# Optimization experiments

Hardware: AMD Instinct MI355X
Metric: run time of the kernel (lower is better)

The kernel has to match this reference:

```python
import jax, jax.numpy as jnp
import numpy as np

H = 8          # num_heads
DK = 64        # head dim (head_size // num_heads)
SPARSITY = 0.5 # pre-softmax random drop probability
DROPOUT = 0.1  # post-softmax dropout probability


def setup_inputs() -> dict:
    key = jax.random.key(0)
    ks = jax.random.split(key, 12)
    B, S, D = 4, 2048, 512
    mk = lambda k, shp, scale=1.0: (jax.random.normal(k, shp, dtype=jnp.float32) * scale)
    return {
        "query": mk(ks[0], (B, S, D)),
        "key": mk(ks[1], (B, S, D)),
        "value": mk(ks[2], (B, S, D)),
        "Wq": mk(ks[3], (D, D), 0.04),
        "bq": mk(ks[4], (D,), 0.02),
        "Wk": mk(ks[5], (D, D), 0.04),
        "bk": mk(ks[6], (D,), 0.02),
        "Wv": mk(ks[7], (D, D), 0.04),
        "bv": mk(ks[8], (D,), 0.02),
        "Wo": mk(ks[9], (D, D), 0.04),
        "bo": mk(ks[10], (D,), 0.02),
    }


def _split_heads(x, B):
    # [B, S, H*DK] -> [B, H, S, DK]
    return x.reshape(B, -1, H, DK).transpose(0, 2, 1, 3)


def reference(query, key, value, Wq, bq, Wk, bk, Wv, bv, Wo, bo):
    B, S, D = query.shape
    # q/k/v projections (torch Linear: x @ W.T + b)
    q = _split_heads(query @ Wq.T + bq, B)   # [B, H, S, DK]
    k = _split_heads(key @ Wk.T + bk, B)
    v = _split_heads(value @ Wv.T + bv, B)

    scores = jnp.einsum("bhqd,bhkd->bhqk", q, k) / jnp.sqrt(jnp.float32(DK))

    # random pre-softmax sparsity mask: keep where U(0,1) > sparsity
    mkey = jax.random.fold_in(jax.random.key(42), 1)
    keep_sparse = jax.random.uniform(mkey, scores.shape) > SPARSITY
    scores = jnp.where(keep_sparse, scores, -jnp.inf)

    p_attn = jax.nn.softmax(scores, axis=-1)

    # dropout on attention probs, inverted scaling as in torch
    dkey = jax.random.fold_in(jax.random.key(42), 2)
    keep_drop = jax.random.uniform(dkey, p_attn.shape) >= DROPOUT
    p_attn = jnp.where(keep_drop, p_attn / (1.0 - DROPOUT), 0.0)

    x = jnp.einsum("bhqk,bhkd->bhqd", p_attn, v)        # [B, H, S, DK]
    x = x.transpose(0, 2, 1, 3).reshape(B, S, H * DK)    # [B, S, D]
    return x @ Wo.T + bo
```

## Files before the change

kernel.cpp:

```cpp
#include <hip/hip_runtime.h>
#include <stdint.h>

#define BATCH  4
#define SQ     2048
#define DMODEL 512
#define NH     8
#define DK     64

typedef __attribute__((ext_vector_type(8))) short short8;
typedef __attribute__((ext_vector_type(4))) float f32x4;

struct TFK { uint32_t a, b; };
constexpr uint32_t rotl_ce(uint32_t x, int d) {
  return (x << d) | (x >> (32 - d));
}
constexpr TFK tf_ce(uint32_t k0, uint32_t k1, uint32_t x0, uint32_t x1) {
  const uint32_t ks[3] = {k0, k1, k0 ^ k1 ^ 0x1BD11BDAu};
  const int rot[2][4] = {{13, 15, 26, 6}, {17, 29, 16, 24}};
  x0 += k0; x1 += k1;
  for (int c = 0; c < 5; ++c) {
    for (int j = 0; j < 4; ++j) {
      x0 += x1; x1 = rotl_ce(x1, rot[c & 1][j]); x1 ^= x0;
    }
    x0 += ks[(c + 1) % 3];
    x1 += ks[(c + 2) % 3] + (uint32_t)(c + 1);
  }
  return TFK{x0, x1};
}
constexpr TFK SPK = tf_ce(0u, 42u, 0u, 1u);
constexpr TFK DPK = tf_ce(0u, 42u, 0u, 2u);

template <uint32_t K0, uint32_t K1>
__device__ __forceinline__ uint32_t tf_bits(uint32_t ctr) {
  constexpr uint32_t KS2 = K0 ^ K1 ^ 0x1BD11BDAu;
  uint32_t x0 = K0;
  uint32_t x1 = K1 + ctr;
#define RND(d) { x0 += x1; x1 = __builtin_amdgcn_alignbit(x1, x1, 32 - (d)); x1 ^= x0; }
  RND(13) RND(15) RND(26) RND(6)
  x0 += K1; x1 += KS2 + 1u;
  RND(17) RND(29) RND(16) RND(24)
  x0 += KS2; x1 += K0 + 2u;
  RND(13) RND(15) RND(26) RND(6)
  x0 += K0; x1 += K1 + 3u;
  RND(17) RND(29) RND(16) RND(24)
  x0 += K1; x1 += KS2 + 4u;
  RND(13) RND(15) RND(26) RND(6)
  x0 += KS2; x1 += K0 + 5u;
#undef RND
  return x0 ^ x1;
}

#define SP_THR 0x80000200u
#define DP_THR 0x1999A200u

__device__ __forceinline__ ushort f2bf_rne(float f) {
  uint32_t u = __float_as_uint(f);
  return (ushort)((u + 0x7fffu + ((u >> 16) & 1u)) >> 16);
}

#define BM 64
#define BN 64
#define BK 32
template <int MODE>
__global__ __launch_bounds__(256) void proj_gemm_t(const float *__restrict__ X,
                                                   const float *__restrict__ W,
                                                   const float *__restrict__ bias,
                                                   void *__restrict__ Yv) {
  __shared__ __align__(16) uint8_t smem[17408];
  float (*Xs)[BM + 4] = (float (*)[BM + 4])smem;
  float (*Ws)[BN + 4] = (float (*)[BN + 4])(smem + 8704);
  const int bm = blockIdx.y * BM;
  const int bn = blockIdx.x * BN;
  const int tid = threadIdx.x;
  const int tx = tid & 15, ty = tid >> 4;
  float acc[4][4] = {};
  const int kk = tid & 31;
  const int r0 = tid >> 5;
  for (int k0 = 0; k0 < DMODEL; k0 += BK) {
#pragma unroll
    for (int p = 0; p < 8; ++p) {
      int r = r0 + p * 8;
      Xs[kk][r] = X[(size_t)(bm + r) * DMODEL + k0 + kk];
      Ws[kk][r] = W[(size_t)(bn + r) * DMODEL + k0 + kk];
    }
    __syncthreads();
#pragma unroll
    for (int k = 0; k < BK; ++k) {
      float4 a = *reinterpret_cast<const float4 *>(&Xs[k][ty * 4]);
      float4 b = *reinterpret_cast<const float4 *>(&Ws[k][tx * 4]);
      float av[4] = {a.x, a.y, a.z, a.w};
      float bv[4] = {b.x, b.y, b.z, b.w};
#pragma unroll
      for (int i = 0; i < 4; ++i)
#pragma unroll
        for (int j = 0; j < 4; ++j) acc[i][j] += av[i] * bv[j];
    }
    __syncthreads();
  }

  if (MODE == 0) {
    float *Y = (float *)Yv;
#pragma unroll
    for (int i = 0; i < 4; ++i) {
      const int m = bm + ty * 4 + i;
#pragma unroll
      for (int j = 0; j < 4; ++j) {
        const int n = bn + tx * 4 + j;
        Y[(size_t)m * DMODEL + n] = acc[i][j] + bias[n];
      }
    }
  } else if (MODE == 1) {
    ushort *Y = (ushort *)Yv;
#pragma unroll
    for (int i = 0; i < 4; ++i) {
      const int m = bm + ty * 4 + i;
      uint32_t u0 = f2bf_rne(acc[i][0] + bias[bn + tx * 4 + 0]);
      uint32_t u1 = f2bf_rne(acc[i][1] + bias[bn + tx * 4 + 1]);
      uint32_t u2 = f2bf_rne(acc[i][2] + bias[bn + tx * 4 + 2]);
      uint32_t u3 = f2bf_rne(acc[i][3] + bias[bn + tx * 4 + 3]);
      uint2 pk;
      pk.x = u0 | (u1 << 16);
      pk.y = u2 | (u3 << 16);
      *(uint2 *)&Y[(size_t)m * DMODEL + bn + tx * 4] = pk;
    }
  } else {
    ushort *T = (ushort *)smem;
#pragma unroll
    for (int i = 0; i < 4; ++i)
#pragma unroll
      for (int j = 0; j < 4; ++j) {
        const int nl = tx * 4 + j, ml = ty * 4 + i;
        T[nl * 72 + ml] = f2bf_rne(acc[i][j] + bias[bn + nl]);
      }
    __syncthreads();
    ushort *Y = (ushort *)Yv;
    const int row = tid >> 2, seg = tid & 3;
    uint4 a = *(uint4 *)&T[row * 72 + seg * 16];
    uint4 b2 = *(uint4 *)&T[row * 72 + seg * 16 + 8];
    const size_t gaddr =
        ((size_t)((bm >> 11) * 512 + bn + row)) * SQ + (bm & 2047) + seg * 16;
    *(uint4 *)&Y[gaddr] = a;
    *(uint4 *)&Y[gaddr + 8] = b2;
  }
}

__global__ __launch_bounds__(256, 2) void attn_mfma(
    const ushort *__restrict__ qp, const ushort *__restrict__ kp,
    const ushort *__restrict__ vpt, float *__restrict__ xa) {
  __shared__ __align__(16) uint8_t lds[24576];
  uint8_t *Ks = lds;
  uint8_t *Vt = lds + 8192;
  const int b = blockIdx.z, h = blockIdx.y;
  const int qb = blockIdx.x * 64;
  const int tid = threadIdx.x;
  const int w = tid >> 6, l = tid & 63;
  const int lr = l & 15, lq = l >> 4;
  uint8_t *Ps = lds + 16384 + w * 2048;
  const int bh = b * NH + h;

  short8 qf[2];
  {
    const int qrow = qb + w * 16 + lr;
    const ushort *qrowp = qp + ((size_t)(b * SQ + qrow)) * DMODEL + h * DK;
    qf[0] = *(const short8 *)(qrowp + lq * 8);
    qf[1] = *(const short8 *)(qrowp + 32 + lq * 8);
  }
  f32x4 o[4];
  f32x4 lacc;
#pragma unroll
  for (int nd = 0; nd < 4; ++nd) o[nd] = (f32x4){0.f, 0.f, 0.f, 0.f};
  lacc = (f32x4){0.f, 0.f, 0.f, 0.f};

  uint32_t rowflat[4];
#pragma unroll
  for (int r = 0; r < 4; ++r)
    rowflat[r] = ((uint32_t)(bh * SQ + qb + w * 16 + lq * 4 + r)) << 11;

  for (int kv = 0; kv < SQ; kv += 64) {
    __syncthreads();
    {
      const int row = tid >> 2;
      const int c0 = (tid & 3) * 2;
      const int sw = (row & 7) << 4;
      const ushort *ksrc =
          kp + ((size_t)(b * SQ + kv + row)) * DMODEL + h * DK + c0 * 8;
      uint4 d0 = *(const uint4 *)ksrc;
      uint4 d1 = *(const uint4 *)(ksrc + 8);
      *(uint4 *)(Ks + ((row * 128 + c0 * 16) ^ sw)) = d0;
      *(uint4 *)(Ks + ((row * 128 + (c0 + 1) * 16) ^ sw)) = d1;
      const ushort *vsrc = vpt + ((size_t)(bh * DK + row)) * SQ + kv + c0 * 8;
      uint4 e0 = *(const uint4 *)vsrc;
      uint4 e1 = *(const uint4 *)(vsrc + 8);
      *(uint4 *)(Vt + ((row * 128 + c0 * 16) ^ sw)) = e0;
      *(uint4 *)(Vt + ((row * 128 + (c0 + 1) * 16) ^ sw)) = e1;
    }
    __syncthreads();

    f32x4 s[4];
#pragma unroll
    for (int ni = 0; ni < 4; ++ni) s[ni] = (f32x4){0.f, 0.f, 0.f, 0.f};
#pragma unroll
    for (int ni = 0; ni < 4; ++ni) {
      const int krow = ni * 16 + lr;
      const int sw = (krow & 7) << 4;
#pragma unroll
      for (int kf = 0; kf < 2; ++kf) {
        short8 kb =
            *(const short8 *)(Ks + ((krow * 128 + kf * 64 + lq * 16) ^ sw));
        s[ni] = __builtin_amdgcn_mfma_f32_16x16x32_bf16(qf[kf], kb, s[ni], 0, 0, 0);
      }
    }

#pragma unroll
    for (int ni = 0; ni < 4; ++ni) {
#pragma unroll
      for (int r = 0; r < 4; ++r) {
        const uint32_t ctr = rowflat[r] + (uint32_t)(kv + ni * 16 + lr);
        const bool keep_s = tf_bits<SPK.a, SPK.b>(ctr) >= SP_THR;
        const bool keep_d = tf_bits<DPK.a, DPK.b>(ctr) >= DP_THR;
        float e = __expf(s[ni][r] * 0.125f);
        float p = keep_s ? e : 0.0f;
        lacc[r] += p;
        float pd = keep_d ? p * (1.0f / 0.9f) : 0.0f;
        const int prow = lq * 4 + r;
        *(ushort *)(Ps + ((prow * 128 + (ni * 16 + lr) * 2) ^ ((prow & 7) << 4))) =
            f2bf_rne(pd);
      }
    }

#pragma unroll
    for (int kf = 0; kf < 2; ++kf) {
      short8 pa = *(const short8 *)(Ps +
                                    ((lr * 128 + kf * 64 + lq * 16) ^ ((lr & 7) << 4)));
#pragma unroll
      for (int nd = 0; nd < 4; ++nd) {
        const int vrow = nd * 16 + lr;
        short8 vb = *(const short8 *)(Vt + ((vrow * 128 + kf * 64 + lq * 16) ^
                                            ((vrow & 7) << 4)));
        o[nd] = __builtin_amdgcn_mfma_f32_16x16x32_bf16(pa, vb, o[nd], 0, 0, 0);
      }
    }
  }

  float inv[4];
#pragma unroll
  for (int r = 0; r < 4; ++r) {
    float t = lacc[r];
    t += __shfl_xor(t, 1);
    t += __shfl_xor(t, 2);
    t += __shfl_xor(t, 4);
    t += __shfl_xor(t, 8);
    inv[r] = 1.0f / t;
  }
#pragma unroll
  for (int nd = 0; nd < 4; ++nd)
#pragma unroll
    for (int r = 0; r < 4; ++r) {
      const int qrow = qb + w * 16 + lq * 4 + r;
      xa[((size_t)(b * SQ + qrow)) * DMODEL + h * DK + nd * 16 + lr] =
          o[nd][r] * inv[r];
    }
}

extern "C" void kernel_launch(void *const *d_in, const int *in_sizes, int n_in,
                              void *d_out, int out_size, void *d_ws,
                              size_t ws_size, hipStream_t stream) {
  (void)in_sizes; (void)n_in; (void)out_size;
  const float *query = (const float *)d_in[0];
  const float *key_  = (const float *)d_in[1];
  const float *value = (const float *)d_in[2];
  const float *Wq = (const float *)d_in[3];
  const float *bq = (const float *)d_in[4];
  const float *Wk = (const float *)d_in[5];
  const float *bk = (const float *)d_in[6];
  const float *Wv = (const float *)d_in[7];
  const float *bv = (const float *)d_in[8];
  const float *Wo = (const float *)d_in[9];
  const float *bo = (const float *)d_in[10];
  float *out = (float *)d_out;

  const size_t MB = (size_t)1 << 20;
  if (ws_size < 40 * MB) return;

  char *ws = (char *)d_ws;
  ushort *qp  = (ushort *)(ws);
  ushort *kp  = (ushort *)(ws + 8 * MB);
  ushort *vpt = (ushort *)(ws + 16 * MB);
  float  *xa  = (float *)(ws + 24 * MB);

  dim3 gg(DMODEL / BN, (BATCH * SQ) / BM);
  proj_gemm_t<1><<<gg, 256, 0, stream>>>(query, Wq, bq, (void *)qp);
  proj_gemm_t<1><<<gg, 256, 0, stream>>>(key_, Wk, bk, (void *)kp);
  proj_gemm_t<2><<<gg, 256, 0, stream>>>(value, Wv, bv, (void *)vpt);

  attn_mfma<<<dim3(SQ / 64, NH, BATCH), 256, 0, stream>>>(qp, kp, vpt, xa);

  proj_gemm_t<0><<<gg, 256, 0, stream>>>(xa, Wo, bo, out);
}
```

Baseline: 794.0 us.

## Use split-bf16 MFMA GEMMs for projections instead of FP32 SIMT GEMMs

Replaces the four FP32 LDS-tiled SIMT projection GEMMs with MFMA bf16 GEMMs. Each FP32 operand is split into a high and a low bf16 part, and three MFMAs per tile approximate FP32 accuracy. New pre-pass kernels split the inputs and weights into these parts, and the attention kernel now writes its output as hi/lo bf16 pairs. The V projection is computed transposed by swapping operands. This adds extra memory traffic for the split passes and loads fragments straight from global memory without LDS staging.

```diff
diff --git a/kernel.cpp b/kernel.cpp
--- a/kernel.cpp
+++ b/kernel.cpp
@@ -57,96 +57,139 @@
   uint32_t u = __float_as_uint(f);
   return (ushort)((u + 0x7fffu + ((u >> 16) & 1u)) >> 16);
 }
-
-#define BM 64
-#define BN 64
-#define BK 32
+__device__ __forceinline__ float bf2f(ushort h) {
+  return __uint_as_float((uint32_t)h << 16);
+}
+
+__device__ __forceinline__ void split4(const float *__restrict__ src,
+                                       ushort *__restrict__ dh,
+                                       ushort *__restrict__ dl, size_t base) {
+  float4 x = *(const float4 *)(src + base);
+  uint32_t h[4], lo[4];
+#pragma unroll
+  for (int i = 0; i < 4; ++i) {
+    float xi = ((const float *)&x)[i];
+    ushort hh = f2bf_rne(xi);
+    h[i] = hh;
+    lo[i] = f2bf_rne(xi - bf2f(hh));
+  }
+  uint2 ph, pl;
+  ph.x = h[0] | (h[1] << 16);  ph.y = h[2] | (h[3] << 16);
+  pl.x = lo[0] | (lo[1] << 16); pl.y = lo[2] | (lo[3] << 16);
+  *(uint2 *)(dh + base) = ph;
+  *(uint2 *)(dl + base) = pl;
+}
+
+__global__ __launch_bounds__(256) void split_inputs_k(
+    const float *__restrict__ q, const float *__restrict__ k,
+    const float *__restrict__ v, ushort *__restrict__ qh,
+    ushort *__restrict__ ql, ushort *__restrict__ kh, ushort *__restrict__ kl,
+    ushort *__restrict__ vh, ushort *__restrict__ vl) {
+  const float *src = blockIdx.y == 0 ? q : (blockIdx.y == 1 ? k : v);
+  ushort *dh = blockIdx.y == 0 ? qh : (blockIdx.y == 1 ? kh : vh);
+  ushort *dl = blockIdx.y == 0 ? ql : (blockIdx.y == 1 ? kl : vl);
+  const size_t base = ((size_t)blockIdx.x * 256 + threadIdx.x) * 4;
+  split4(src, dh, dl, base);
+}
+
+__global__ __launch_bounds__(256) void split_w_k(
+    const float *__restrict__ w0, const float *__restrict__ w1,
+    const float *__restrict__ w2, const float *__restrict__ w3,
+    ushort *__restrict__ h0, ushort *__restrict__ l0, ushort *__restrict__ h1,
+    ushort *__restrict__ l1, ushort *__restrict__ h2, ushort *__restrict__ l2,
+    ushort *__restrict__ h3, ushort *__restrict__ l3) {
+  const int y = blockIdx.y;
+  const float *src = y == 0 ? w0 : (y == 1 ? w1 : (y == 2 ? w2 : w3));
+  ushort *dh = y == 0 ? h0 : (y == 1 ? h1 : (y == 2 ? h2 : h3));
+  ushort *dl = y == 0 ? l0 : (y == 1 ? l1 : (y == 2 ? l2 : l3));
+  const size_t base = ((size_t)blockIdx.x * 256 + threadIdx.x) * 4;
+  split4(src, dh, dl, base);
+}
+
 template <int MODE>
-__global__ __launch_bounds__(256) void proj_gemm_t(const float *__restrict__ X,
-                                                   const float *__restrict__ W,
-                                                   const float *__restrict__ bias,
-                                                   void *__restrict__ Yv) {
-  __shared__ __align__(16) uint8_t smem[17408];
-  float (*Xs)[BM + 4] = (float (*)[BM + 4])smem;
-  float (*Ws)[BN + 4] = (float (*)[BN + 4])(smem + 8704);
-  const int bm = blockIdx.y * BM;
-  const int bn = blockIdx.x * BN;
+__global__ __launch_bounds__(256) void proj_mfma(
+    const ushort *__restrict__ Ah, const ushort *__restrict__ Al,
+    const ushort *__restrict__ Bh, const ushort *__restrict__ Bl,
+    const float *__restrict__ bias, void *__restrict__ Yv) {
   const int tid = threadIdx.x;
-  const int tx = tid & 15, ty = tid >> 4;
-  float acc[4][4] = {};
-  const int kk = tid & 31;
-  const int r0 = tid >> 5;
-  for (int k0 = 0; k0 < DMODEL; k0 += BK) {
-#pragma unroll
-    for (int p = 0; p < 8; ++p) {
-      int r = r0 + p * 8;
-      Xs[kk][r] = X[(size_t)(bm + r) * DMODEL + k0 + kk];
-      Ws[kk][r] = W[(size_t)(bn + r) * DMODEL + k0 + kk];
-    }
-    __syncthreads();
-#pragma unroll
-    for (int k = 0; k < BK; ++k) {
-      float4 a = *reinterpret_cast<const float4 *>(&Xs[k][ty * 4]);
-      float4 b = *reinterpret_cast<const float4 *>(&Ws[k][tx * 4]);
-      float av[4] = {a.x, a.y, a.z, a.w};
-      float bv[4] = {b.x, b.y, b.z, b.w};
-#pragma unroll
-      for (int i = 0; i < 4; ++i)
-#pragma unroll
-        for (int j = 0; j < 4; ++j) acc[i][j] += av[i] * bv[j];
-    }
-    __syncthreads();
-  }
-
-  if (MODE == 0) {
-    float *Y = (float *)Yv;
-#pragma unroll
-    for (int i = 0; i < 4; ++i) {
-      const int m = bm + ty * 4 + i;
-#pragma unroll
-      for (int j = 0; j < 4; ++j) {
-        const int n = bn + tx * 4 + j;
-        Y[(size_t)m * DMODEL + n] = acc[i][j] + bias[n];
-      }
-    }
-  } else if (MODE == 1) {
-    ushort *Y = (ushort *)Yv;
-#pragma unroll
-    for (int i = 0; i < 4; ++i) {
-      const int m = bm + ty * 4 + i;
-      uint32_t u0 = f2bf_rne(acc[i][0] + bias[bn + tx * 4 + 0]);
-      uint32_t u1 = f2bf_rne(acc[i][1] + bias[bn + tx * 4 + 1]);
-      uint32_t u2 = f2bf_rne(acc[i][2] + bias[bn + tx * 4 + 2]);
-      uint32_t u3 = f2bf_rne(acc[i][3] + bias[bn + tx * 4 + 3]);
-      uint2 pk;
-      pk.x = u0 | (u1 << 16);
-      pk.y = u2 | (u3 << 16);
-      *(uint2 *)&Y[(size_t)m * DMODEL + bn + tx * 4] = pk;
-    }
-  } else {
-    ushort *T = (ushort *)smem;
-#pragma unroll
-    for (int i = 0; i < 4; ++i)
-#pragma unroll
-      for (int j = 0; j < 4; ++j) {
-        const int nl = tx * 4 + j, ml = ty * 4 + i;
-        T[nl * 72 + ml] = f2bf_rne(acc[i][j] + bias[bn + nl]);
-      }
-    __syncthreads();
-    ushort *Y = (ushort *)Yv;
-    const int row = tid >> 2, seg = tid & 3;
-    uint4 a = *(uint4 *)&T[row * 72 + seg * 16];
-    uint4 b2 = *(uint4 *)&T[row * 72 + seg * 16 + 8];
-    const size_t gaddr =
-        ((size_t)((bm >> 11) * 512 + bn + row)) * SQ + (bm & 2047) + seg * 16;
-    *(uint4 *)&Y[gaddr] = a;
-    *(uint4 *)&Y[gaddr + 8] = b2;
-  }
+  const int w = tid >> 6, l = tid & 63;
+  const int lr = l & 15, lq = l >> 4;
+  const int am = blockIdx.y * 128 + w * 32;
+  const int bn = blockIdx.x * 64;
+  f32x4 acc[2][4];
+#pragma unroll
+  for (int i = 0; i < 2; ++i)
+#pragma unroll
+    for (int j = 0; j < 4; ++j) acc[i][j] = (f32x4){0.f, 0.f, 0.f, 0.f};
+
+#pragma unroll 2
+  for (int k0 = 0; k0 < DMODEL; k0 += 32) {
+    short8 ah[2], al[2], bh[4], bl[4];
+#pragma unroll
+    for (int mf = 0; mf < 2; ++mf) {
+      const size_t off = (size_t)(am + mf * 16 + lr) * DMODEL + k0 + lq * 8;
+      ah[mf] = *(const short8 *)(Ah + off);
+      al[mf] = *(const short8 *)(Al + off);
+    }
+#pragma unroll
+    for (int nf = 0; nf < 4; ++nf) {
+      const size_t off = (size_t)(bn + nf * 16 + lr) * DMODEL + k0 + lq * 8;
+      bh[nf] = *(const short8 *)(Bh + off);
+      bl[nf] = *(const short8 *)(Bl + off);
+    }
+#pragma unroll
+    for (int mf = 0; mf < 2; ++mf)
+#pragma unroll
+      for (int nf = 0; nf < 4; ++nf) {
+        acc[mf][nf] = __builtin_amdgcn_mfma_f32_16x16x32_bf16(
+            ah[mf], bh[nf], acc[mf][nf], 0, 0, 0);
+        acc[mf][nf] = __builtin_amdgcn_mfma_f32_16x16x32_bf16(
+            ah[mf], bl[nf], acc[mf][nf], 0, 0, 0);
+        acc[mf][nf] = __builtin_amdgcn_mfma_f32_16x16x32_bf16(
+            al[mf], bh[nf], acc[mf][nf], 0, 0, 0);
+      }
+  }
+
+#pragma unroll
+  for (int mf = 0; mf < 2; ++mf)
+#pragma unroll
+    for (int nf = 0; nf < 4; ++nf) {
+      if (MODE == 0) {
+        float *Y = (float *)Yv;
+        const int gn = bn + nf * 16 + lr;
+        const float bb = bias[gn];
+#pragma unroll
+        for (int r = 0; r < 4; ++r) {
+          const int gm = am + mf * 16 + lq * 4 + r;
+          Y[(size_t)gm * DMODEL + gn] = acc[mf][nf][r] + bb;
+        }
+      } else if (MODE == 1) {
+        ushort *Y = (ushort *)Yv;
+        const int gn = bn + nf * 16 + lr;
+        const float bb = bias[gn];
+#pragma unroll
+        for (int r = 0; r < 4; ++r) {
+          const int gm = am + mf * 16 + lq * 4 + r;
+          Y[(size_t)gm * DMODEL + gn] = f2bf_rne(acc[mf][nf][r] + bb);
+        }
+      } else {
+        ushort *Y = (ushort *)Yv;
+        const int gm2 = bn + nf * 16 + lr;
+        const int bcol = gm2 >> 11, scol = gm2 & 2047;
+#pragma unroll
+        for (int r = 0; r < 4; ++r) {
+          const int gn2 = am + mf * 16 + lq * 4 + r;
+          Y[((size_t)(bcol * DMODEL + gn2)) * SQ + scol] =
+              f2bf_rne(acc[mf][nf][r] + bias[gn2]);
+        }
+      }
+    }
 }
 
 __global__ __launch_bounds__(256, 2) void attn_mfma(
     const ushort *__restrict__ qp, const ushort *__restrict__ kp,
-    const ushort *__restrict__ vpt, float *__restrict__ xa) {
+    const ushort *__restrict__ vpt, ushort *__restrict__ xah,
+    ushort *__restrict__ xal) {
   __shared__ __align__(16) uint8_t lds[24576];
   uint8_t *Ks = lds;
   uint8_t *Vt = lds + 8192;
@@ -257,8 +300,12 @@
 #pragma unroll
     for (int r = 0; r < 4; ++r) {
       const int qrow = qb + w * 16 + lq * 4 + r;
-      xa[((size_t)(b * SQ + qrow)) * DMODEL + h * DK + nd * 16 + lr] =
-          o[nd][r] * inv[r];
+      const size_t idx =
+          ((size_t)(b * SQ + qrow)) * DMODEL + h * DK + nd * 16 + lr;
+      const float val = o[nd][r] * inv[r];
+      const ushort hh = f2bf_rne(val);
+      xah[idx] = hh;
+      xal[idx] = f2bf_rne(val - bf2f(hh));
     }
 }
 
@@ -280,20 +327,40 @@
   float *out = (float *)d_out;
 
   const size_t MB = (size_t)1 << 20;
-  if (ws_size < 40 * MB) return;
+  if (ws_size < 92 * MB) return;
 
   char *ws = (char *)d_ws;
-  ushort *qp  = (ushort *)(ws);
-  ushort *kp  = (ushort *)(ws + 8 * MB);
-  ushort *vpt = (ushort *)(ws + 16 * MB);
-  float  *xa  = (float *)(ws + 24 * MB);
-
-  dim3 gg(DMODEL / BN, (BATCH * SQ) / BM);
-  proj_gemm_t<1><<<gg, 256, 0, stream>>>(query, Wq, bq, (void *)qp);
-  proj_gemm_t<1><<<gg, 256, 0, stream>>>(key_, Wk, bk, (void *)kp);
-  proj_gemm_t<2><<<gg, 256, 0, stream>>>(value, Wv, bv, (void *)vpt);
-
-  attn_mfma<<<dim3(SQ / 64, NH, BATCH), 256, 0, stream>>>(qp, kp, vpt, xa);
-
-  proj_gemm_t<0><<<gg, 256, 0, stream>>>(xa, Wo, bo, out);
-}
+  ushort *qih = (ushort *)(ws);
+  ushort *qil = (ushort *)(ws + 8 * MB);
+  ushort *kih = (ushort *)(ws + 16 * MB);
+  ushort *kil = (ushort *)(ws + 24 * MB);
+  ushort *vih = (ushort *)(ws + 32 * MB);
+  ushort *vil = (ushort *)(ws + 40 * MB);
+  ushort *Wqh = (ushort *)(ws + 48 * MB);
+  ushort *Wql = (ushort *)(ws + 48 * MB + 512 * 1024);
+  ushort *Wkh = (ushort *)(ws + 49 * MB);
+  ushort *Wkl = (ushort *)(ws + 49 * MB + 512 * 1024);
+  ushort *Wvh = (ushort *)(ws + 50 * MB);
+  ushort *Wvl = (ushort *)(ws + 50 * MB + 512 * 1024);
+  ushort *Woh = (ushort *)(ws + 51 * MB);
+  ushort *Wol = (ushort *)(ws + 51 * MB + 512 * 1024);
+  ushort *qp  = (ushort *)(ws + 52 * MB);
+  ushort *kp  = (ushort *)(ws + 60 * MB);
+  ushort *vpt = (ushort *)(ws + 68 * MB);
+  ushort *xah = (ushort *)(ws + 76 * MB);
+  ushort *xal = (ushort *)(ws + 84 * MB);
+
+  split_inputs_k<<<dim3(4096, 3), 256, 0, stream>>>(query, key_, value, qih,
+                                                    qil, kih, kil, vih, vil);
+  split_w_k<<<dim3(256, 4), 256, 0, stream>>>(Wq, Wk, Wv, Wo, Wqh, Wql, Wkh,
+                                              Wkl, Wvh, Wvl, Woh, Wol);
+
+  proj_mfma<1><<<dim3(8, 64), 256, 0, stream>>>(qih, qil, Wqh, Wql, bq, qp);
+  proj_mfma<1><<<dim3(8, 64), 256, 0, stream>>>(kih, kil, Wkh, Wkl, bk, kp);
+  proj_mfma<2><<<dim3(128, 4), 256, 0, stream>>>(Wvh, Wvl, vih, vil, bv, vpt);
+
+  attn_mfma<<<dim3(SQ / 64, NH, BATCH), 256, 0, stream>>>(qp, kp, vpt, xah,
+                                                          xal);
+
+  proj_mfma<0><<<dim3(8, 64), 256, 0, stream>>>(xah, xal, Woh, Wol, bo, out);
+}
```

After: 721.6 us. -9.1%, faster.
